# Kernel optimization log

Measured on AMD Instinct MI355X. Metric: run time of the kernel, lower is better.

## Reference

```python
import jax, jax.numpy as jnp
import numpy as np

B, D, F, E, G = 2048, 1024, 4096, 16, 2
EPS = 1e-9
LN_EPS = 1e-5


def setup_inputs() -> dict:
    key = jax.random.key(0)
    ks = jax.random.split(key, 10)
    s_in = 1.0 / np.sqrt(D)
    s_out = 1.0 / np.sqrt(F)
    return {
        "cycle_curve_data": jax.random.normal(ks[0], (B, D), jnp.float32),
        "logits": jax.random.normal(ks[1], (B, E), jnp.float32),
        "moe_masks": jax.random.randint(ks[2], (B, E), 0, 2, jnp.int32),
        "ew_in": jax.random.uniform(ks[3], (E, D, F), jnp.float32, -s_in, s_in),
        "ew_out": jax.random.uniform(ks[4], (E, F, D), jnp.float32, -s_out, s_out),
        "eb_out": jax.random.uniform(ks[5], (E, D), jnp.float32, -s_out, s_out),
        "gw_in": jax.random.uniform(ks[6], (G, D, F), jnp.float32, -s_in, s_in),
        "gw_out": jax.random.uniform(ks[7], (G, F, D), jnp.float32, -s_out, s_out),
        "gb_out": jax.random.uniform(ks[8], (G, D), jnp.float32, -s_out, s_out),
        "ln_gamma": jnp.ones((D,), jnp.float32),
        "ln_beta": jnp.zeros((D,), jnp.float32),
    }


def _moe_forward(x, logits, moe_masks, ew_in, ew_out, eb_out, gw_in, gw_out, gb_out, ln_gamma, ln_beta):
    b = x.shape[0]
    mask = (moe_masks == 1).astype(logits.dtype)          # [B,E]
    raw = jax.nn.softmax(logits, axis=1)                   # [B,E]
    gates = raw * mask
    gates = gates / (jnp.sum(gates, axis=1, keepdims=True) + EPS)
    # Per-expert MLPBlockGELU over all tokens; gate=0 zeroes out non-dispatched
    # tokens exactly as MOEDispatcher.combine does.
    h = jax.nn.gelu(jnp.einsum('bd,edf->ebf', x, ew_in), approximate=False)  # [E,B,F]
    eout = jnp.einsum('ebf,efd->ebd', h, ew_out) + eb_out[:, None, :]        # [E,B,D]
    moe_out = jnp.einsum('be,ebd->bd', gates, eout).astype(jnp.bfloat16)     # combine + bf16 cast
    # general experts (dense, added to routed output; bf16+f32 promotes to f32)
    gh = jax.nn.gelu(jnp.einsum('bd,gdf->gbf', x, gw_in), approximate=False)
    gout = jnp.einsum('gbf,gfd->gbd', gh, gw_out) + gb_out[:, None, :]       # [G,B,D]
    final = jnp.sum(gout, axis=0) + moe_out                                  # f32
    # residual + LayerNorm
    y = final + x
    mu = jnp.mean(y, axis=-1, keepdims=True)
    var = jnp.mean(jnp.square(y - mu), axis=-1, keepdims=True)
    final_out = (y - mu) * jax.lax.rsqrt(var + LN_EPS) * ln_gamma + ln_beta
    # training losses
    expert_logits = jnp.mean(raw, axis=0)                                    # [E]
    expert_sample_count = jnp.sum((gates != 0).astype(raw.dtype), axis=0) / b
    aug_loss = jnp.mean(expert_logits * expert_sample_count)
    s = jnp.sum(raw * mask) / b
    guide_loss = (1.0 - s) * (1.0 - s)
    return final_out, aug_loss, guide_loss


def reference(cycle_curve_data, logits, moe_masks, ew_in, ew_out, eb_out, gw_in, gw_out, gb_out, ln_gamma, ln_beta):
    return _moe_forward(cycle_curve_data, logits, moe_masks, ew_in, ew_out, eb_out,
                        gw_in, gw_out, gb_out, ln_gamma, ln_beta)
```

## Files before the change

kernel.cpp:

```cpp
#include <hip/hip_runtime.h>
#include <hip/hip_bf16.h>

#define B_TOK 2048
#define DDIM 1024
#define FDIM 4096
#define NE 16
#define NG 2
#define BD ((long)B_TOK * DDIM)

typedef unsigned short u16;
typedef __attribute__((ext_vector_type(8))) short bf16x8;
typedef __attribute__((ext_vector_type(4))) float f32x4;

__device__ inline u16 f2bf(float x) {
  union { float f; unsigned u; } v; v.f = x;
  return (u16)((v.u + 0x7fffu + ((v.u >> 16) & 1u)) >> 16);
}
__device__ inline float bfround(float x) {
  union { float f; unsigned u; } v; v.f = x;
  v.u = ((v.u + 0x7fffu + ((v.u >> 16) & 1u)) >> 16) << 16;
  return v.f;
}
__device__ inline float gelu_exact(float x) {
  return 0.5f * x * (1.0f + erff(x * 0.70710678118654752440f));
}
__device__ inline void gload16(const void* g, void* l) {
  __builtin_amdgcn_global_load_lds((const __attribute__((address_space(1))) void*)g,
                                   (__attribute__((address_space(3))) void*)l, 16, 0, 0);
}
__device__ inline float waveSum(float v) {
  v += __shfl_down(v, 32); v += __shfl_down(v, 16); v += __shfl_down(v, 8);
  v += __shfl_down(v, 4);  v += __shfl_down(v, 2);  v += __shfl_down(v, 1);
  return v;
}

__global__ __launch_bounds__(256) void gating_kernel(
    const float* __restrict__ logits, const int* __restrict__ masks,
    float* __restrict__ gates, float* __restrict__ loss)
{
  const int b = blockIdx.x * 256 + threadIdx.x;
  const int lane = threadIdx.x & 63;
  const float* lr = logits + (long)b * NE;
  const int*   mr = masks  + (long)b * NE;
  float raw[NE]; int mk[NE];
  float mx = -1e30f;
#pragma unroll
  for (int e = 0; e < NE; ++e) { raw[e] = lr[e]; mx = fmaxf(mx, raw[e]); }
  float s = 0.f;
#pragma unroll
  for (int e = 0; e < NE; ++e) { raw[e] = expf(raw[e] - mx); s += raw[e]; }
  float inv = 1.0f / s;
#pragma unroll
  for (int e = 0; e < NE; ++e) raw[e] *= inv;
  float gs = 0.f;
#pragma unroll
  for (int e = 0; e < NE; ++e) { mk[e] = (mr[e] == 1); gs += mk[e] ? raw[e] : 0.f; }
  float ginv = 1.0f / (gs + 1e-9f);
  float* gr = gates + (long)b * NE;
#pragma unroll
  for (int e = 0; e < NE; ++e) gr[e] = (mk[e] ? raw[e] : 0.f) * ginv;
#pragma unroll
  for (int e = 0; e < NE; ++e) {
    float cs = waveSum(raw[e]);
    float cc = waveSum(mk[e] ? 1.f : 0.f);
    if (lane == 0) { atomicAdd(&loss[e], cs); atomicAdd(&loss[NE + e], cc); }
  }
  float t = waveSum(gs);
  if (lane == 0) atomicAdd(&loss[32], t);
}

__global__ void finalize_loss(const float* __restrict__ loss, float* __restrict__ out2) {
  if (threadIdx.x == 0) {
    float aug = 0.f;
    for (int e = 0; e < NE; ++e)
      aug += (loss[e] / (float)B_TOK) * (loss[NE + e] / (float)B_TOK);
    aug *= (1.0f / NE);
    float s = loss[32] / (float)B_TOK;
    out2[0] = aug;
    out2[1] = (1.f - s) * (1.f - s);
  }
}

__global__ __launch_bounds__(256) void compact_kernel(
    const int* __restrict__ masks, int* __restrict__ tok,
    int* __restrict__ pos, int* __restrict__ cnts)
{
  const int e = blockIdx.x, tid = threadIdx.x;
  const int lane = tid & 63, wave = tid >> 6;
  __shared__ int wcnt[4];
  __shared__ int runbase;
  if (tid == 0) runbase = 0;
  __syncthreads();
  for (int b0 = 0; b0 < B_TOK; b0 += 256) {
    int b = b0 + tid;
    int m = (masks[(long)b * NE + e] == 1);
    unsigned long long bal = __ballot(m);
    int pre = __popcll(bal & ((1ull << lane) - 1ull));
    if (lane == 0) wcnt[wave] = __popcll(bal);
    __syncthreads();
    int base = runbase;
    for (int w = 0; w < wave; ++w) base += wcnt[w];
    if (m) {
      int p = base + pre;
      tok[(e << 11) + p] = b;
      pos[(long)b * NE + e] = p;
    } else {
      pos[(long)b * NE + e] = -1;
    }
    __syncthreads();
    if (tid == 0) runbase += wcnt[0] + wcnt[1] + wcnt[2] + wcnt[3];
    __syncthreads();
  }
  const int cnt = runbase;
  const int cnt_pad = (cnt + 127) & ~127;
  for (int i = cnt + tid; i < cnt_pad; i += 256)
    tok[(e << 11) + i] = 0;
  if (tid == 0) { cnts[e] = cnt; cnts[NE + e] = cnt_pad; }
}

__global__ __launch_bounds__(256) void cvt_x_kernel(const float* __restrict__ x, u16* __restrict__ xb) {
  long i = ((long)blockIdx.x * 256 + threadIdx.x) * 4;
  float4 v = *(const float4*)&x[i];
  ushort4 o; o.x = f2bf(v.x); o.y = f2bf(v.y); o.z = f2bf(v.z); o.w = f2bf(v.w);
  *(ushort4*)&xb[i] = o;
}

__global__ __launch_bounds__(256) void bias_init_kernel(
    const float* __restrict__ gates, const float* __restrict__ eb,
    const float* __restrict__ gb, float* __restrict__ moe_bias, float* __restrict__ gen_p)
{
  long i = (long)blockIdx.x * 256 + threadIdx.x;
  int b = (int)(i >> 10), d = (int)(i & 1023);
  const float* gr = gates + (long)b * NE;
  float s = 0.f;
#pragma unroll
  for (int e = 0; e < NE; ++e) s += gr[e] * eb[e * DDIM + d];
  moe_bias[i] = s;
  gen_p[i] = gb[d] + gb[DDIM + d];
#pragma unroll
  for (int sl = 1; sl < 8; ++sl) gen_p[sl * BD + i] = 0.f;
}

__global__ __launch_bounds__(256) void transpose_cvt(
    const float* __restrict__ src, u16* __restrict__ dst,
    int R, int C, long sZ, long dZ)
{
  __shared__ float t[64][65];
  const float* s = src + (long)blockIdx.z * sZ;
  u16* d = dst + (long)blockIdx.z * dZ;
  const int c0 = blockIdx.x * 64, r0 = blockIdx.y * 64;
  const int tid = threadIdx.x;
#pragma unroll
  for (int it = 0; it < 4; ++it) {
    int idx = tid + it * 256;
    int r = idx >> 4, cq = (idx & 15) * 4;
    float4 v = *(const float4*)&s[(long)(r0 + r) * C + c0 + cq];
    t[r][cq] = v.x; t[r][cq + 1] = v.y; t[r][cq + 2] = v.z; t[r][cq + 3] = v.w;
  }
  __syncthreads();
#pragma unroll
  for (int it = 0; it < 4; ++it) {
    int idx = tid + it * 256;
    int c = idx >> 4, rq = (idx & 15) * 4;
    ushort4 o;
    o.x = f2bf(t[rq][c]); o.y = f2bf(t[rq+1][c]); o.z = f2bf(t[rq+2][c]); o.w = f2bf(t[rq+3][c]);
    *(ushort4*)&d[(long)(c0 + c) * R + r0 + rq] = o;
  }
}

template<int MODE>
__global__ __launch_bounds__(256) void gemm128(
    const u16* __restrict__ A, int lda, long aZ,
    const u16* __restrict__ Bm, int ldb, long bZ,
    int klen,
    u16* __restrict__ H, long hZ,
    float* __restrict__ C, long cZ,
    const int* __restrict__ tok, const int* __restrict__ cnts, int ebase)
{
  int lin = ((int)blockIdx.z * gridDim.y + blockIdx.y) * gridDim.x + blockIdx.x;
  const int T = gridDim.x * gridDim.y * gridDim.z;
  lin = (lin & 7) * (T >> 3) + (lin >> 3);
  const int bx = lin % gridDim.x;
  const int rest = lin / gridDim.x;
  const int by = rest % gridDim.y;
  const int bz = rest / gridDim.y;

  const int zi = (MODE == 2) ? (bz >> 2) : bz;
  const int ks = (MODE == 2) ? (bz & 3) * klen : 0;
  const int m0 = by * 128, n0 = bx * 128;
  if (MODE != 2 && cnts && m0 >= cnts[NE + ebase + zi]) return;

  __shared__ u16 sA[128 * 32];
  __shared__ u16 sB[128 * 32];
  const u16* Az = A + (long)zi * aZ;
  const u16* Bz = Bm + (long)zi * bZ;
  const int tid = threadIdx.x, lane = tid & 63, wave = tid >> 6;

  const int off = tid * 16;
  const int sr  = off >> 6;
  const int ske = (off & 63) >> 1;
  int arow0 = m0 + sr, arow1 = m0 + sr + 64;
  if (MODE == 0 && tok) {
    const int* tz = tok + ((ebase + zi) << 11);
    arow0 = tz[arow0]; arow1 = tz[arow1];
  }
  const u16* gA0 = Az + (long)arow0 * lda + ks + ske;
  const u16* gA1 = Az + (long)arow1 * lda + ks + ske;
  const u16* gB0 = Bz + (long)(n0 + sr) * ldb + ks + ske;
  const u16* gB1 = gB0 + (long)64 * ldb;
  u16* lA0 = &sA[wave * 512];
  u16* lA1 = &sA[2048 + wave * 512];
  u16* lB0 = &sB[wave * 512];
  u16* lB1 = &sB[2048 + wave * 512];

  const int wr = wave >> 1, wc = wave & 1;
  const int fr = lane & 15, fk = (lane >> 4) * 8;
  const u16* rA = &sA[(wr * 64 + fr) * 32 + fk];
  const u16* rB = &sB[(wc * 64 + fr) * 32 + fk];

  f32x4 zero = {0.f, 0.f, 0.f, 0.f};
  f32x4 acc[4][4];
#pragma unroll
  for (int m = 0; m < 4; ++m)
#pragma unroll
    for (int n = 0; n < 4; ++n) acc[m][n] = zero;

  for (int kk = 0; kk < klen; kk += 32) {
    gload16(gA0 + kk, lA0);
    gload16(gA1 + kk, lA1);
    gload16(gB0 + kk, lB0);
    gload16(gB1 + kk, lB1);
    __syncthreads();
    bf16x8 av[4], bv[4];
#pragma unroll
    for (int m = 0; m < 4; ++m) av[m] = *(const bf16x8*)(rA + m * 512);
#pragma unroll
    for (int n = 0; n < 4; ++n) bv[n] = *(const bf16x8*)(rB + n * 512);
#pragma unroll
    for (int m = 0; m < 4; ++m)
#pragma unroll
      for (int n = 0; n < 4; ++n)
        acc[m][n] = __builtin_amdgcn_mfma_f32_16x16x32_bf16(av[m], bv[n], acc[m][n], 0, 0, 0);
    __syncthreads();
  }

  const int er = m0 + wr * 64 + (lane >> 4) * 4;
  const int ec = n0 + wc * 64 + fr;
  if (MODE == 0) {
    u16* Hz = H + (long)zi * hZ;
#pragma unroll
    for (int m = 0; m < 4; ++m)
#pragma unroll
      for (int n = 0; n < 4; ++n) {
        f32x4 v = acc[m][n];
        int rb = er + m * 16, cb = ec + n * 16;
#pragma unroll
        for (int j = 0; j < 4; ++j)
          Hz[(long)(rb + j) * FDIM + cb] = f2bf(gelu_exact(v[j]));
      }
  } else if (MODE == 1) {
    float* Cz = C + (long)(ebase + zi) * cZ;
#pragma unroll
    for (int m = 0; m < 4; ++m)
#pragma unroll
      for (int n = 0; n < 4; ++n) {
        f32x4 v = acc[m][n];
        int rb = er + m * 16, cb = ec + n * 16;
#pragma unroll
        for (int j = 0; j < 4; ++j)
          Cz[(long)(rb + j) * DDIM + cb] = v[j];
      }
  } else {
    float* Cz = C + (long)bz * cZ;
#pragma unroll
    for (int m = 0; m < 4; ++m)
#pragma unroll
      for (int n = 0; n < 4; ++n) {
        f32x4 v = acc[m][n];
        int rb = er + m * 16, cb = ec + n * 16;
#pragma unroll
        for (int j = 0; j < 4; ++j)
          Cz[(long)(rb + j) * DDIM + cb] += v[j];
      }
  }
}

__global__ __launch_bounds__(256) void combine_ln_kernel(
    const float* __restrict__ x, const float* __restrict__ moe_bias,
    const float* __restrict__ Eout, const float* __restrict__ gen_p,
    const int* __restrict__ pos, const float* __restrict__ gates,
    const float* __restrict__ gamma, const float* __restrict__ beta,
    float* __restrict__ out)
{
  const int b = blockIdx.x, tid = threadIdx.x;
  const int lane = tid & 63, wave = tid >> 6;
  const long base = (long)b * DDIM;
  __shared__ int posr[NE];
  __shared__ float gr[NE];
  __shared__ float red[4];
  if (tid < NE) { posr[tid] = pos[(long)b * NE + tid]; gr[tid] = gates[(long)b * NE + tid]; }
  __syncthreads();
  float y[4];
  float ls = 0.f;
#pragma unroll
  for (int i = 0; i < 4; ++i) {
    int d = tid + i * 256;
    long idx = base + d;
    float moe = moe_bias[idx];
#pragma unroll
    for (int e = 0; e < NE; ++e) {
      int p = posr[e];
      if (p >= 0) moe += gr[e] * Eout[((long)e * B_TOK + p) * DDIM + d];
    }
    moe = bfround(moe);
    float ge = 0.f;
#pragma unroll
    for (int sl = 0; sl < 8; ++sl) ge += gen_p[(long)sl * BD + idx];
    y[i] = moe + ge + x[idx];
    ls += y[i];
  }
  float t = waveSum(ls);
  if (lane == 0) red[wave] = t;
  __syncthreads();
  float mean = (red[0] + red[1] + red[2] + red[3]) * (1.0f / DDIM);
  __syncthreads();
  float vs = 0.f;
#pragma unroll
  for (int i = 0; i < 4; ++i) { float d2 = y[i] - mean; vs += d2 * d2; }
  t = waveSum(vs);
  if (lane == 0) red[wave] = t;
  __syncthreads();
  float var = (red[0] + red[1] + red[2] + red[3]) * (1.0f / DDIM);
  float inv = rsqrtf(var + 1e-5f);
#pragma unroll
  for (int i = 0; i < 4; ++i) {
    int d = tid + i * 256;
    out[base + d] = (y[i] - mean) * inv * gamma[d] + beta[d];
  }
}

extern "C" void kernel_launch(void* const* d_in, const int* in_sizes, int n_in,
                              void* d_out, int out_size, void* d_ws, size_t ws_size,
                              hipStream_t stream)
{
  const float* x      = (const float*)d_in[0];
  const float* logits = (const float*)d_in[1];
  const int*   masks  = (const int*)d_in[2];
  const float* ew_in  = (const float*)d_in[3];
  const float* ew_out = (const float*)d_in[4];
  const float* eb_out = (const float*)d_in[5];
  const float* gw_in  = (const float*)d_in[6];
  const float* gw_out = (const float*)d_in[7];
  const float* gb_out = (const float*)d_in[8];
  const float* gamma  = (const float*)d_in[9];
  const float* beta   = (const float*)d_in[10];
  float* out = (float*)d_out;

  char* w = (char*)d_ws;
  size_t off = 0;
  auto alloc = [&](size_t bytes) -> void* {
    off = (off + 4095) & ~(size_t)4095;
    void* p = w + off; off += bytes; return p;
  };
  const long DF = (long)DDIM * FDIM;
  const long BF = (long)B_TOK * FDIM;

  float* gates    = (float*)alloc((size_t)B_TOK * NE * 4);
  float* loss     = (float*)alloc(64 * 4);
  int*   tok      = (int*)alloc((size_t)NE * B_TOK * 4);
  int*   pos      = (int*)alloc((size_t)B_TOK * NE * 4);
  int*   cnts     = (int*)alloc(2 * NE * 4);
  u16*   xb       = (u16*)alloc((size_t)BD * 2);
  float* moe_bias = (float*)alloc((size_t)BD * 4);
  float* gen_p    = (float*)alloc(8 * (size_t)BD * 4);
  float* Eout     = (float*)alloc((size_t)NE * BD * 4);
  u16*   WgInT    = (u16*)alloc((size_t)NG * DF * 2);
  u16*   WgOutT   = (u16*)alloc((size_t)NG * DF * 2);
  u16*   Hg       = (u16*)alloc((size_t)NG * BF * 2);

  const size_t per = 2 * (size_t)DF * 2 + (size_t)BF * 2 + 3 * 4096;
  int CE = 16;
  while (CE > 1 && off + (size_t)CE * per > ws_size) CE >>= 1;
  u16* WinT  = (u16*)alloc((size_t)CE * DF * 2);
  u16* WoutT = (u16*)alloc((size_t)CE * DF * 2);
  u16* Hb    = (u16*)alloc((size_t)CE * BF * 2);

  hipMemsetAsync(loss, 0, 64 * 4, stream);
  gating_kernel<<<8, 256, 0, stream>>>(logits, masks, gates, loss);
  finalize_loss<<<1, 64, 0, stream>>>(loss, out + BD);
  compact_kernel<<<NE, 256, 0, stream>>>(masks, tok, pos, cnts);
  cvt_x_kernel<<<2048, 256, 0, stream>>>(x, xb);
  bias_init_kernel<<<8192, 256, 0, stream>>>(gates, eb_out, gb_out, moe_bias, gen_p);

  for (int e0 = 0; e0 < NE; e0 += CE) {
    transpose_cvt<<<dim3(FDIM/64, DDIM/64, CE), 256, 0, stream>>>(
        ew_in + (long)e0 * DF, WinT, DDIM, FDIM, DF, DF);
    transpose_cvt<<<dim3(DDIM/64, FDIM/64, CE), 256, 0, stream>>>(
        ew_out + (long)e0 * DF, WoutT, FDIM, DDIM, DF, DF);
    gemm128<0><<<dim3(FDIM/128, B_TOK/128, CE), 256, 0, stream>>>(
        xb, DDIM, 0L, WinT, DDIM, DF, DDIM,
        Hb, BF, nullptr, 0L, tok, cnts, e0);
    gemm128<1><<<dim3(DDIM/128, B_TOK/128, CE), 256, 0, stream>>>(
        Hb, FDIM, BF, WoutT, FDIM, DF, FDIM,
        nullptr, 0L, Eout, BD, nullptr, cnts, e0);
  }

  transpose_cvt<<<dim3(FDIM/64, DDIM/64, NG), 256, 0, stream>>>(
      gw_in, WgInT, DDIM, FDIM, DF, DF);
  transpose_cvt<<<dim3(DDIM/64, FDIM/64, NG), 256, 0, stream>>>(
      gw_out, WgOutT, FDIM, DDIM, DF, DF);
  gemm128<0><<<dim3(FDIM/128, B_TOK/128, NG), 256, 0, stream>>>(
      xb, DDIM, 0L, WgInT, DDIM, DF, DDIM,
      Hg, BF, nullptr, 0L, nullptr, nullptr, 0);
  gemm128<2><<<dim3(DDIM/128, B_TOK/128, NG * 4), 256, 0, stream>>>(
      Hg, FDIM, BF, WgOutT, FDIM, DF, FDIM / 4,
      nullptr, 0L, gen_p, BD, nullptr, nullptr, 0);

  combine_ln_kernel<<<B_TOK, 256, 0, stream>>>(
      x, moe_bias, Eout, gen_p, pos, gates, gamma, beta, out);
}
```

Before: 923.2 us.

## Double-buffer LDS tiles in GEMM and use polynomial erf for GELU

The GEMM main loop now keeps two LDS buffers per operand, so the global-to-LDS load for the next K tile is issued while MFMAs run on the current one, which removes one barrier-bound stall per iteration. GELU's erff is replaced with the Abramowitz-Stegun polynomial approximation using a hardware reciprocal and __expf, making the epilogue cheaper. The approximation has an absolute error of about 1e-7, and the loop assumes an even tile count, since it always stages buffer 1 without a bounds check. LDS use per block doubles.

After: 929.4 us. Within noise of the previous version (+0.7%).

```diff
diff --git a/kernel.cpp b/kernel.cpp
--- a/kernel.cpp
+++ b/kernel.cpp
@@ -21,8 +21,16 @@
   v.u = ((v.u + 0x7fffu + ((v.u >> 16) & 1u)) >> 16) << 16;
   return v.f;
 }
+__device__ inline float fast_erf(float x) {
+  float ax = fabsf(x);
+  float t = __builtin_amdgcn_rcpf(1.0f + 0.3275911f * ax);
+  float poly = t * (0.254829592f + t * (-0.284496736f + t * (1.421413741f +
+               t * (-1.453152027f + t * 1.061405429f))));
+  float r = 1.0f - poly * __expf(-ax * ax);
+  return copysignf(r, x);
+}
 __device__ inline float gelu_exact(float x) {
-  return 0.5f * x * (1.0f + erff(x * 0.70710678118654752440f));
+  return 0.5f * x * (1.0f + fast_erf(x * 0.70710678118654752440f));
 }
 __device__ inline void gload16(const void* g, void* l) {
   __builtin_amdgcn_global_load_lds((const __attribute__((address_space(1))) void*)g,
@@ -190,8 +198,8 @@
   const int m0 = by * 128, n0 = bx * 128;
   if (MODE != 2 && cnts && m0 >= cnts[NE + ebase + zi]) return;
 
-  __shared__ u16 sA[128 * 32];
-  __shared__ u16 sB[128 * 32];
+  __shared__ u16 sA[2][128 * 32];
+  __shared__ u16 sB[2][128 * 32];
   const u16* Az = A + (long)zi * aZ;
   const u16* Bz = Bm + (long)zi * bZ;
   const int tid = threadIdx.x, lane = tid & 63, wave = tid >> 6;
@@ -208,15 +216,11 @@
   const u16* gA1 = Az + (long)arow1 * lda + ks + ske;
   const u16* gB0 = Bz + (long)(n0 + sr) * ldb + ks + ske;
   const u16* gB1 = gB0 + (long)64 * ldb;
-  u16* lA0 = &sA[wave * 512];
-  u16* lA1 = &sA[2048 + wave * 512];
-  u16* lB0 = &sB[wave * 512];
-  u16* lB1 = &sB[2048 + wave * 512];
 
   const int wr = wave >> 1, wc = wave & 1;
   const int fr = lane & 15, fk = (lane >> 4) * 8;
-  const u16* rA = &sA[(wr * 64 + fr) * 32 + fk];
-  const u16* rB = &sB[(wc * 64 + fr) * 32 + fk];
+  const int rAo = (wr * 64 + fr) * 32 + fk;
+  const int rBo = (wc * 64 + fr) * 32 + fk;
 
   f32x4 zero = {0.f, 0.f, 0.f, 0.f};
   f32x4 acc[4][4];
@@ -225,22 +229,34 @@
 #pragma unroll
     for (int n = 0; n < 4; ++n) acc[m][n] = zero;
 
-  for (int kk = 0; kk < klen; kk += 32) {
-    gload16(gA0 + kk, lA0);
-    gload16(gA1 + kk, lA1);
-    gload16(gB0 + kk, lB0);
-    gload16(gB1 + kk, lB1);
-    __syncthreads();
+  auto STAGE = [&](int buf, int kk) {
+    gload16(gA0 + kk, &sA[buf][wave * 512]);
+    gload16(gA1 + kk, &sA[buf][2048 + wave * 512]);
+    gload16(gB0 + kk, &sB[buf][wave * 512]);
+    gload16(gB1 + kk, &sB[buf][2048 + wave * 512]);
+  };
+  auto COMPUTE = [&](int buf) {
     bf16x8 av[4], bv[4];
 #pragma unroll
-    for (int m = 0; m < 4; ++m) av[m] = *(const bf16x8*)(rA + m * 512);
-#pragma unroll
-    for (int n = 0; n < 4; ++n) bv[n] = *(const bf16x8*)(rB + n * 512);
+    for (int m = 0; m < 4; ++m) av[m] = *(const bf16x8*)(&sA[buf][rAo + m * 512]);
+#pragma unroll
+    for (int n = 0; n < 4; ++n) bv[n] = *(const bf16x8*)(&sB[buf][rBo + n * 512]);
 #pragma unroll
     for (int m = 0; m < 4; ++m)
 #pragma unroll
       for (int n = 0; n < 4; ++n)
         acc[m][n] = __builtin_amdgcn_mfma_f32_16x16x32_bf16(av[m], bv[n], acc[m][n], 0, 0, 0);
+  };
+
+  const int nt = klen >> 5;
+  STAGE(0, 0);
+  __syncthreads();
+  for (int t = 0; t < nt; t += 2) {
+    STAGE(1, (t + 1) << 5);
+    COMPUTE(0);
+    __syncthreads();
+    if (t + 2 < nt) STAGE(0, (t + 2) << 5);
+    COMPUTE(1);
     __syncthreads();
   }
 
```
